# Kernel tuning notes

Hardware: AMD Instinct MI355X
Metric: run time of the kernel (lower is better)

## Reference

```python
import jax, jax.numpy as jnp
import numpy as np

NUM_PEAK = 28000
NUM_GENE = 12000
N_NODES = NUM_PEAK + NUM_GENE
N_EDGES = 640000
NUM_TOPICS = 100
T_HIDDEN = 512
EMB = 64
HID = 128  # 2 * emb_size, hidden_channels of GCN
BATCH = 256
BN_EPS = 1e-5


def setup_inputs() -> dict:
    key = jax.random.key(0)
    ks = iter(jax.random.split(key, 64))
    def nrm(shape, s=0.05):
        return jax.random.normal(next(ks), shape, dtype=jnp.float32) * s
    def unif(shape):
        return jax.random.uniform(next(ks), shape, dtype=jnp.float32)
    z = lambda *s: jnp.zeros(s, jnp.float32)
    o = lambda *s: jnp.ones(s, jnp.float32)
    inp = dict(
        Gene=unif((BATCH, NUM_GENE)),
        Gene_normalized=unif((BATCH, NUM_GENE)),
        Peak=unif((BATCH, NUM_PEAK)),
        Peak_normalized=unif((BATCH, NUM_PEAK)),
        feature_matrix=nrm((N_NODES, EMB), 1.0),
        # GATv2 layer 1 (EMB -> HID, heads=1)
        Wl1=nrm((HID, EMB)), bl1=z(HID), Wr1=nrm((HID, EMB)), br1=z(HID),
        att1=nrm((HID,), 0.1), bias1=z(HID),
        # GATv2 layer 2 (HID -> EMB)
        Wl2=nrm((EMB, HID)), bl2=z(EMB), Wr2=nrm((EMB, HID)), br2=z(EMB),
        att2=nrm((EMB,), 0.1), bias2=z(EMB),
        # gene encoder: Linear + ReLU + BN + Linear + ReLU + BN
        gW1=nrm((T_HIDDEN, NUM_GENE)), gb1=z(T_HIDDEN), gg1=o(T_HIDDEN), gbe1=z(T_HIDDEN),
        gW2=nrm((T_HIDDEN, T_HIDDEN)), gb2=z(T_HIDDEN), gg2=o(T_HIDDEN), gbe2=z(T_HIDDEN),
        # peak encoder
        pW1=nrm((T_HIDDEN, NUM_PEAK)), pb1=z(T_HIDDEN), pg1=o(T_HIDDEN), pbe1=z(T_HIDDEN),
        pW2=nrm((T_HIDDEN, T_HIDDEN)), pb2=z(T_HIDDEN), pg2=o(T_HIDDEN), pbe2=z(T_HIDDEN),
        mu_W=nrm((NUM_TOPICS, T_HIDDEN)), mu_b=z(NUM_TOPICS),
        ls_W=nrm((NUM_TOPICS, T_HIDDEN)), ls_b=z(NUM_TOPICS),
        alphas_W=nrm((NUM_TOPICS, EMB)),
        alphas_star_W=nrm((NUM_TOPICS, EMB)),
        edge_index=jax.random.randint(next(ks), (2, N_EDGES), 0, N_NODES),
    )
    return inp


def _batchnorm(h, gamma, beta):
    # training-style BN over batch axis (biased variance), eps=1e-5
    m = h.mean(axis=0)
    v = jnp.mean((h - m) ** 2, axis=0)
    return (h - m) * jax.lax.rsqrt(v + BN_EPS) * gamma + beta


def _gatv2(x, src, dst, Wl, bl, Wr, br, att, bias):
    # PyG GATv2Conv, heads=1: e_ij = att . leaky_relu(Wl x_j + Wr x_i),
    # softmax over incoming edges of i, out_i = sum_j alpha_ij * (Wl x_j) + bias
    xl = x @ Wl.T + bl            # [N, C]
    xr = x @ Wr.T + br            # [N, C]
    e = jax.nn.leaky_relu(xl[src] + xr[dst], negative_slope=0.2)  # [E, C]
    logit = e @ att               # [E]
    m = jax.ops.segment_max(logit, dst, num_segments=N_NODES)
    ex = jnp.exp(logit - m[dst])
    den = jax.ops.segment_sum(ex, dst, num_segments=N_NODES)
    alpha = ex / (den[dst] + 1e-16)
    out = jax.ops.segment_sum(alpha[:, None] * xl[src], dst, num_segments=N_NODES)
    return out + bias


def _encode(x, W1, b1, g1, be1, W2, b2, g2, be2, mu_W, mu_b, ls_W, ls_b):
    h = _batchnorm(jax.nn.relu(x @ W1.T + b1), g1, be1)
    h = _batchnorm(jax.nn.relu(h @ W2.T + b2), g2, be2)
    mu = h @ mu_W.T + mu_b
    logsigma = 2.0 * (h @ ls_W.T + ls_b)
    kl = -0.5 * jnp.sum(1.0 + logsigma - mu ** 2 - jnp.exp(logsigma), axis=-1).mean()
    return mu, kl


def reference(Gene, Gene_normalized, Peak, Peak_normalized, feature_matrix,
              Wl1, bl1, Wr1, br1, att1, bias1,
              Wl2, bl2, Wr2, br2, att2, bias2,
              gW1, gb1, gg1, gbe1, gW2, gb2, gg2, gbe2,
              pW1, pb1, pg1, pbe1, pW2, pb2, pg2, pbe2,
              mu_W, mu_b, ls_W, ls_b, alphas_W, alphas_star_W, edge_index):
    # ---- variational encoders (eval mode: dropout off, theta from mu) ----
    mu_d, kl_d = _encode(Gene_normalized, gW1, gb1, gg1, gbe1, gW2, gb2, gg2, gbe2,
                         mu_W, mu_b, ls_W, ls_b)
    mu_j, kl_j = _encode(Peak_normalized, pW1, pb1, pg1, pbe1, pW2, pb2, pg2, pbe2,
                         mu_W, mu_b, ls_W, ls_b)
    theta_d = jax.nn.softmax(mu_d, axis=-1)   # [B, K]
    theta_j = jax.nn.softmax(mu_j, axis=-1)
    kld_theta = kl_d + kl_j

    # ---- GCN embedding: two GATv2Conv layers with self-loops ----
    loops = jnp.arange(N_NODES)
    src = jnp.concatenate([edge_index[0], loops])
    dst = jnp.concatenate([edge_index[1], loops])
    h = jax.nn.relu(_gatv2(feature_matrix, src, dst, Wl1, bl1, Wr1, br1, att1, bias1))
    emb = _gatv2(h, src, dst, Wl2, bl2, Wr2, br2, att2, bias2)
    emb = jax.nn.relu(emb)  # theta_act applied in forward
    eta_matrix = emb[:NUM_PEAK]   # [num_peak, EMB]
    rho_matrix = emb[NUM_PEAK:]   # [num_gene, EMB]

    # ---- topic-word matrices: softmax over genes/peaks (dim=0), transposed ----
    beta_gene = jax.nn.softmax(rho_matrix @ alphas_W.T, axis=0).T        # [K, num_gene]
    beta_peak = jax.nn.softmax(eta_matrix @ alphas_star_W.T, axis=0).T   # [K, num_peak]

    # ---- decode + reconstruction loss ----
    preds_gene = jnp.log(theta_d @ beta_gene + 1e-6)
    preds_peak = jnp.log(theta_j @ beta_peak + 1e-6)
    recon = (-(preds_gene * Gene).sum(-1) - (preds_peak * Peak).sum(-1)).mean()
    return recon, kld_theta
```

## Files before the change

### kernel.cpp

```cpp
#include <hip/hip_runtime.h>
#include <cstdint>
#include <cstddef>

using u16 = unsigned short;
using u32 = unsigned int;
typedef __attribute__((ext_vector_type(8))) short bf16x8;
typedef __attribute__((ext_vector_type(4))) float f32x4;

static constexpr int NUM_PEAK = 28000;
static constexpr int NUM_GENE = 12000;
static constexpr int N_NODES  = NUM_PEAK + NUM_GENE;
static constexpr int N_EDGES  = 640000;
static constexpr int E_TOTAL  = N_EDGES + N_NODES;
static constexpr int NT       = 100;
static constexpr int NT2      = 200;
static constexpr int NTP      = 128;
static constexpr int TH       = 512;
static constexpr int EMB      = 64;
static constexpr int HID      = 128;
static constexpr int BATCH    = 256;
static constexpr int SCAN_CHUNK = 1024;
static constexpr int SCAN_NB  = (N_NODES + SCAN_CHUNK - 1) / SCAN_CHUNK;
static constexpr int ENC_CH   = 640;
static constexpr int KPG      = 12032;
static constexpr int KPP      = 28032;
#define BN_EPS 1e-5f

__device__ __forceinline__ u16 f2bf(float f) {
  u32 b = __float_as_uint(f);
  return (u16)((b + 0x7FFFu + ((b >> 16) & 1u)) >> 16);
}
__device__ __forceinline__ float bf2f(u16 u) {
  return __uint_as_float((u32)u << 16);
}
__device__ __forceinline__ u32 f2o(float f) {
  u32 u = __float_as_uint(f);
  return (u & 0x80000000u) ? ~u : (u | 0x80000000u);
}
__device__ __forceinline__ float o2f(u32 u) {
  return (u & 0x80000000u) ? __uint_as_float(u & 0x7fffffffu) : __uint_as_float(~u);
}

struct CvtJobs {
  const float* src[12];
  u16* dst[12];
  u32 n[12];
  u32 start[12];
  int count;
};

__global__ __launch_bounds__(256) void cvt_all(CvtJobs J) {
  const int bid = blockIdx.x;
  int seg = 0;
  while (seg + 1 < J.count && bid >= (int)J.start[seg + 1]) ++seg;
  const float* __restrict__ src = J.src[seg];
  u16* __restrict__ dst = J.dst[seg];
  const u32 n = J.n[seg];
  const u32 i = (u32)(bid - J.start[seg]) * 2048u + threadIdx.x * 8u;
  if (i + 8 <= n) {
    float4 a = *(const float4*)(src + i);
    float4 b = *(const float4*)(src + i + 4);
    ushort4 o0{f2bf(a.x), f2bf(a.y), f2bf(a.z), f2bf(a.w)};
    ushort4 o1{f2bf(b.x), f2bf(b.y), f2bf(b.z), f2bf(b.w)};
    *(ushort4*)(dst + i) = o0;
    *(ushort4*)(dst + i + 4) = o1;
  } else {
    for (u32 j = i; j < n; ++j) dst[j] = f2bf(src[j]);
  }
}

__global__ __launch_bounds__(256) void cvt_pad(
    const float* __restrict__ g, u16* __restrict__ gb,
    const float* __restrict__ p, u16* __restrict__ pb) {
  const bool sec = (blockIdx.y != 0);
  const float* __restrict__ src = sec ? p : g;
  u16* __restrict__ dst = sec ? pb : gb;
  const int K = sec ? NUM_PEAK : NUM_GENE;
  const int Kp = sec ? KPP : KPG;
  const size_t total = (size_t)BATCH * Kp;
  size_t i = ((size_t)blockIdx.x * 256 + threadIdx.x) * 8;
  const size_t stride = (size_t)gridDim.x * 256 * 8;
  for (; i < total; i += stride) {
    const int col = (int)(i % Kp);
    const size_t row = i / Kp;
    ushort4 o0{0, 0, 0, 0}, o1{0, 0, 0, 0};
    if (col + 8 <= K) {
      const float* s = src + row * K + col;
      float4 a = *(const float4*)s;
      float4 b = *(const float4*)(s + 4);
      o0 = ushort4{f2bf(a.x), f2bf(a.y), f2bf(a.z), f2bf(a.w)};
      o1 = ushort4{f2bf(b.x), f2bf(b.y), f2bf(b.z), f2bf(b.w)};
    }
    *(ushort4*)(dst + i) = o0;
    *(ushort4*)(dst + i + 4) = o1;
  }
}

struct GP {
  const u16* A; const u16* B; float* C; u16* Cb; const float* bias;
  int M, N, K, chunk;
};

__global__ __launch_bounds__(256) void gemm_bt_bf16(GP g0, GP g1, int dual) {
  const GP& g = (dual && blockIdx.z) ? g1 : g0;
  const int M = g.M, N = g.N, K = g.K;
  __shared__ u16 As[64][40];
  __shared__ u16 Bs[64][40];
  const int tid = threadIdx.x;
  const int bm = blockIdx.y * 64, bn = blockIdx.x * 64;
  if (bm >= M || bn >= N) return;
  const int k0 = dual ? 0 : blockIdx.z * g.chunk;
  const int k1 = min(K, k0 + g.chunk);
  const int w = tid >> 6, lane = tid & 63;
  const int wm = (w >> 1) * 32, wn = (w & 1) * 32;
  const int fr = lane & 15;
  const int ks = (lane >> 4) * 8;
  const int srow = tid >> 2, sseg = (tid & 3) * 8;
  f32x4 acc[2][2] = {};
  for (int kt = k0; kt < k1; kt += 32) {
    const int gk = kt + sseg;
    {
      const int gm = bm + srow;
      bf16x8 v = {0, 0, 0, 0, 0, 0, 0, 0};
      if (gm < M) {
        if (gk + 8 <= k1) v = *(const bf16x8*)(g.A + (size_t)gm * K + gk);
        else if (gk < k1)
          for (int e = 0; e < k1 - gk; ++e) ((short*)&v)[e] = (short)g.A[(size_t)gm * K + gk + e];
      }
      *(bf16x8*)&As[srow][sseg] = v;
    }
    {
      const int gn = bn + srow;
      bf16x8 v = {0, 0, 0, 0, 0, 0, 0, 0};
      if (gn < N) {
        if (gk + 8 <= k1) v = *(const bf16x8*)(g.B + (size_t)gn * K + gk);
        else if (gk < k1)
          for (int e = 0; e < k1 - gk; ++e) ((short*)&v)[e] = (short)g.B[(size_t)gn * K + gk + e];
      }
      *(bf16x8*)&Bs[srow][sseg] = v;
    }
    __syncthreads();
    bf16x8 a0 = *(const bf16x8*)&As[wm + fr][ks];
    bf16x8 a1 = *(const bf16x8*)&As[wm + 16 + fr][ks];
    bf16x8 b0 = *(const bf16x8*)&Bs[wn + fr][ks];
    bf16x8 b1 = *(const bf16x8*)&Bs[wn + 16 + fr][ks];
    acc[0][0] = __builtin_amdgcn_mfma_f32_16x16x32_bf16(a0, b0, acc[0][0], 0, 0, 0);
    acc[0][1] = __builtin_amdgcn_mfma_f32_16x16x32_bf16(a0, b1, acc[0][1], 0, 0, 0);
    acc[1][0] = __builtin_amdgcn_mfma_f32_16x16x32_bf16(a1, b0, acc[1][0], 0, 0, 0);
    acc[1][1] = __builtin_amdgcn_mfma_f32_16x16x32_bf16(a1, b1, acc[1][1], 0, 0, 0);
    __syncthreads();
  }
  const bool split = (!dual && gridDim.z > 1);
#pragma unroll
  for (int fi = 0; fi < 2; ++fi)
#pragma unroll
    for (int fj = 0; fj < 2; ++fj)
#pragma unroll
      for (int r = 0; r < 4; ++r) {
        const int row = bm + wm + fi * 16 + (lane >> 4) * 4 + r;
        const int col = bn + wn + fj * 16 + fr;
        if (row < M && col < N) {
          const float v = acc[fi][fj][r];
          if (split) atomicAdd(&g.C[(size_t)row * N + col], v);
          else if (g.Cb) g.Cb[(size_t)row * N + col] = f2bf(v + (g.bias ? g.bias[col] : 0.f));
          else g.C[(size_t)row * N + col] = v + (g.bias ? g.bias[col] : 0.f);
        }
      }
}

__device__ __forceinline__ int swz64(int row, int colu16) {
  return row * 64 + ((((colu16 >> 3) ^ row) & 7) << 3) + (colu16 & 7);
}

__global__ __launch_bounds__(256) void gemm_enc1(
    const u16* __restrict__ A0, const float* __restrict__ B0, float* __restrict__ C0,
    int K0, int Kp0, int ksp0,
    const u16* __restrict__ A1, const float* __restrict__ B1, float* __restrict__ C1,
    int K1, int Kp1) {
  const int z = blockIdx.z;
  const bool second = (z >= ksp0);
  const u16* __restrict__ A = second ? A1 : A0;
  const float* __restrict__ B = second ? B1 : B0;
  float* __restrict__ C = second ? C1 : C0;
  const int K = second ? K1 : K0;
  const int Kp = second ? Kp1 : Kp0;
  const int zz = second ? z - ksp0 : z;
  const int k0 = zz * ENC_CH;
  const int k1 = min(K, k0 + ENC_CH);
  __shared__ u16 As[128 * 64];
  __shared__ u16 Bs[64 * 64];
  const int tid = threadIdx.x;
  const int bm = blockIdx.y * 128;
  const int bn = blockIdx.x * 64;
  const int w = tid >> 6, lane = tid & 63;
  const int wm = w * 32;
  const int fr = lane & 15, g = lane >> 4;
  const int ar = tid >> 1, acol = (tid & 1) * 32;
  const int br = tid >> 2, bcol = (tid & 3) * 16;
  const u16* Abase = A + (size_t)(bm + ar) * Kp + acol;
  const float* Bbase = B + (size_t)(bn + br) * K + bcol;

  bf16x8 rA0, rA1, rA2, rA3;
  float4 rB0, rB1, rB2, rB3;
  auto LD = [&](int kt) {
    const u16* sa = Abase + kt;
    rA0 = *(const bf16x8*)(sa);
    rA1 = *(const bf16x8*)(sa + 8);
    rA2 = *(const bf16x8*)(sa + 16);
    rA3 = *(const bf16x8*)(sa + 24);
    if (kt + bcol + 16 <= K) {
      const float* sb = Bbase + kt;
      rB0 = *(const float4*)(sb);
      rB1 = *(const float4*)(sb + 4);
      rB2 = *(const float4*)(sb + 8);
      rB3 = *(const float4*)(sb + 12);
    } else {
      rB0 = float4{0.f, 0.f, 0.f, 0.f}; rB1 = rB0; rB2 = rB0; rB3 = rB0;
    }
  };
  auto ST = [&]() {
    *(bf16x8*)&As[swz64(ar, acol)] = rA0;
    *(bf16x8*)&As[swz64(ar, acol + 8)] = rA1;
    *(bf16x8*)&As[swz64(ar, acol + 16)] = rA2;
    *(bf16x8*)&As[swz64(ar, acol + 24)] = rA3;
    ushort4 p0{f2bf(rB0.x), f2bf(rB0.y), f2bf(rB0.z), f2bf(rB0.w)};
    ushort4 p1{f2bf(rB1.x), f2bf(rB1.y), f2bf(rB1.z), f2bf(rB1.w)};
    ushort4 p2{f2bf(rB2.x), f2bf(rB2.y), f2bf(rB2.z), f2bf(rB2.w)};
    ushort4 p3{f2bf(rB3.x), f2bf(rB3.y), f2bf(rB3.z), f2bf(rB3.w)};
    const int b0 = swz64(br, bcol);
    const int b1 = swz64(br, bcol + 8);
    *(ushort4*)&Bs[b0] = p0;
    *(ushort4*)&Bs[b0 + 4] = p1;
    *(ushort4*)&Bs[b1] = p2;
    *(ushort4*)&Bs[b1 + 4] = p3;
  };

  f32x4 acc[2][4] = {};
  LD(k0);
  ST();
  for (int kt = k0; kt < k1; kt += 64) {
    __syncthreads();
    const bool more = (kt + 64 < k1);
    if (more) LD(kt + 64);
#pragma unroll
    for (int s = 0; s < 2; ++s) {
      const int kc = s * 32 + g * 8;
      bf16x8 bfr[4];
#pragma unroll
      for (int fj = 0; fj < 4; ++fj)
        bfr[fj] = *(const bf16x8*)&Bs[swz64(fj * 16 + fr, kc)];
#pragma unroll
      for (int fi = 0; fi < 2; ++fi) {
        bf16x8 a = *(const bf16x8*)&As[swz64(wm + fi * 16 + fr, kc)];
#pragma unroll
        for (int fj = 0; fj < 4; ++fj)
          acc[fi][fj] = __builtin_amdgcn_mfma_f32_16x16x32_bf16(a, bfr[fj], acc[fi][fj], 0, 0, 0);
      }
    }
    __syncthreads();
    if (more) ST();
  }
#pragma unroll
  for (int fi = 0; fi < 2; ++fi)
#pragma unroll
    for (int fj = 0; fj < 4; ++fj)
#pragma unroll
      for (int r = 0; r < 4; ++r) {
        const int row = bm + wm + fi * 16 + g * 4 + r;
        const int col = bn + fj * 16 + fr;
        atomicAdd(&C[(size_t)row * TH + col], acc[fi][fj][r]);
      }
}

__global__ __launch_bounds__(256) void recon_fused(
    const u16* __restrict__ thg, const u16* __restrict__ betag,
    const float* __restrict__ Xg, int Ng, int tiles_g,
    const u16* __restrict__ thp, const u16* __restrict__ betap,
    const float* __restrict__ Xp, int Np, float* __restrict__ partials) {
  __shared__ float pred[64][65];
  __shared__ float wsum[4];
  int ct = blockIdx.x;
  const u16* A; const u16* B; const float* X; int N;
  if (ct < tiles_g) { A = thg; B = betag; X = Xg; N = Ng; }
  else { ct -= tiles_g; A = thp; B = betap; X = Xp; N = Np; }
  const int bm = blockIdx.y * 64, bn = ct * 64;
  const int tid = threadIdx.x, w = tid >> 6, lane = tid & 63;
  const int wm = (w >> 1) * 32, wn = (w & 1) * 32;
  const int fr = lane & 15, ks = (lane >> 4) * 8;
  const u16* Ar0 = A + (size_t)(bm + wm + fr) * NTP;
  const u16* Ar1 = A + (size_t)(bm + wm + 16 + fr) * NTP;
  bf16x8 a0[4], a1[4];
#pragma unroll
  for (int kt = 0; kt < 4; ++kt) {
    a0[kt] = *(const bf16x8*)(Ar0 + kt * 32 + ks);
    a1[kt] = *(const bf16x8*)(Ar1 + kt * 32 + ks);
  }
  const int gn0 = min(bn + wn + fr, N - 1);
  const int gn1 = min(bn + wn + 16 + fr, N - 1);
  const u16* Br0 = B + (size_t)gn0 * NTP;
  const u16* Br1 = B + (size_t)gn1 * NTP;
  f32x4 acc[2][2] = {};
#pragma unroll
  for (int kt = 0; kt < 4; ++kt) {
    bf16x8 b0 = *(const bf16x8*)(Br0 + kt * 32 + ks);
    bf16x8 b1 = *(const bf16x8*)(Br1 + kt * 32 + ks);
    acc[0][0] = __builtin_amdgcn_mfma_f32_16x16x32_bf16(a0[kt], b0, acc[0][0], 0, 0, 0);
    acc[0][1] = __builtin_amdgcn_mfma_f32_16x16x32_bf16(a0[kt], b1, acc[0][1], 0, 0, 0);
    acc[1][0] = __builtin_amdgcn_mfma_f32_16x16x32_bf16(a1[kt], b0, acc[1][0], 0, 0, 0);
    acc[1][1] = __builtin_amdgcn_mfma_f32_16x16x32_bf16(a1[kt], b1, acc[1][1], 0, 0, 0);
  }
#pragma unroll
  for (int fi = 0; fi < 2; ++fi)
#pragma unroll
    for (int fj = 0; fj < 2; ++fj)
#pragma unroll
      for (int r = 0; r < 4; ++r)
        pred[wm + fi * 16 + (lane >> 4) * 4 + r][wn + fj * 16 + fr] = acc[fi][fj][r];
  __syncthreads();
  float local = 0.f;
  if (bn + 64 <= N) {
#pragma unroll
    for (int k = 0; k < 4; ++k) {
      const int j = k * 1024 + tid * 4;
      const int row = j >> 6, col = j & 63;
      const float4 xv = *(const float4*)(X + (size_t)(bm + row) * N + bn + col);
      local += xv.x * __logf(pred[row][col + 0] + 1e-6f);
      local += xv.y * __logf(pred[row][col + 1] + 1e-6f);
      local += xv.z * __logf(pred[row][col + 2] + 1e-6f);
      local += xv.w * __logf(pred[row][col + 3] + 1e-6f);
    }
  } else {
#pragma unroll
    for (int k = 0; k < 16; ++k) {
      const int idx = k * 256 + tid, row = idx >> 6, col = idx & 63;
      if (bn + col < N)
        local += X[(size_t)(bm + row) * N + bn + col] * __logf(pred[row][col] + 1e-6f);
    }
  }
  for (int o = 32; o > 0; o >>= 1) local += __shfl_down(local, o);
  if (lane == 0) wsum[w] = local;
  __syncthreads();
  if (tid == 0)
    partials[(size_t)blockIdx.y * gridDim.x + blockIdx.x] =
        wsum[0] + wsum[1] + wsum[2] + wsum[3];
}

__global__ __launch_bounds__(256) void final_recon(
    const float* __restrict__ partials, int n, float* __restrict__ out) {
  float s = 0.f;
  for (int i = threadIdx.x; i < n; i += 256) s += partials[i];
  __shared__ float red[256];
  red[threadIdx.x] = s; __syncthreads();
  for (int o = 128; o > 0; o >>= 1) {
    if (threadIdx.x < o) red[threadIdx.x] += red[threadIdx.x + o];
    __syncthreads();
  }
  if (threadIdx.x == 0) out[0] = -red[0] * (1.f / BATCH);
}

__global__ __launch_bounds__(256) void bias_relu_bn2(
    const float* __restrict__ Hg, const float* __restrict__ bg,
    const float* __restrict__ gg, const float* __restrict__ beg,
    u16* __restrict__ og,
    const float* __restrict__ Hp, const float* __restrict__ bp,
    const float* __restrict__ gp, const float* __restrict__ bep,
    u16* __restrict__ op) {
  int c = blockIdx.x;
  const float *H, *b, *gma, *be; u16* ob;
  if (c < TH) { H = Hg; b = bg; gma = gg; be = beg; ob = og; }
  else { c -= TH; H = Hp; b = bp; gma = gp; be = bep; ob = op; }
  const int r = threadIdx.x;
  float v = fmaxf(H[(size_t)r * TH + c] + b[c], 0.f);
  __shared__ float red[BATCH];
  red[r] = v; __syncthreads();
  for (int s = BATCH / 2; s > 0; s >>= 1) { if (r < s) red[r] += red[r + s]; __syncthreads(); }
  const float mean = red[0] * (1.f / BATCH);
  __syncthreads();
  const float d = v - mean;
  red[r] = d * d; __syncthreads();
  for (int s = BATCH / 2; s > 0; s >>= 1) { if (r < s) red[r] += red[r + s]; __syncthreads(); }
  const float var = red[0] * (1.f / BATCH);
  ob[(size_t)r * TH + c] = f2bf(d * rsqrtf(var + BN_EPS) * gma[c] + be[c]);
}

__global__ __launch_bounds__(128) void row_kl_theta(
    const float* __restrict__ mld, const float* __restrict__ mlj,
    const float* __restrict__ mu_b, const float* __restrict__ ls_b,
    u16* __restrict__ thd, u16* __restrict__ thj, float* __restrict__ kl_out) {
  const float* ml = blockIdx.y ? mlj : mld;
  u16* thb = blockIdx.y ? thj : thd;
  const int b = blockIdx.x;
  const int t = threadIdx.x;
  const bool act = (t < NT);
  float mu = 0.f, ls = 0.f, term = 0.f;
  if (act) {
    mu = ml[(size_t)b * NT2 + t] + mu_b[t];
    ls = 2.f * (ml[(size_t)b * NT2 + NT + t] + ls_b[t]);
    term = 1.f + ls - mu * mu - expf(ls);
  }
  __shared__ float red[128];
  red[t] = act ? term : 0.f; __syncthreads();
  for (int s = 64; s > 0; s >>= 1) { if (t < s) red[t] += red[t + s]; __syncthreads(); }
  if (t == 0) atomicAdd(kl_out, -0.5f * red[0] * (1.f / BATCH));
  __syncthreads();
  red[t] = act ? mu : -INFINITY; __syncthreads();
  for (int s = 64; s > 0; s >>= 1) { if (t < s) red[t] = fmaxf(red[t], red[t + s]); __syncthreads(); }
  const float mx = red[0];
  __syncthreads();
  const float e = act ? expf(mu - mx) : 0.f;
  red[t] = e; __syncthreads();
  for (int s = 64; s > 0; s >>= 1) { if (t < s) red[t] += red[t + s]; __syncthreads(); }
  thb[(size_t)b * NTP + t] = act ? f2bf(e / red[0]) : (u16)0;
}

__global__ __launch_bounds__(256) void deg_count(
    const int* __restrict__ ei, int* __restrict__ deg) {
  int e = blockIdx.x * 256 + threadIdx.x;
  if (e >= E_TOTAL) return;
  const int d = (e < N_EDGES) ? ei[N_EDGES + e] : e - N_EDGES;
  atomicAdd(&deg[d], 1);
}

__global__ __launch_bounds__(256) void scan_part(
    const int* __restrict__ deg, int* __restrict__ bsum) {
  const int base = blockIdx.x * SCAN_CHUNK + threadIdx.x * 4;
  int s = 0;
#pragma unroll
  for (int i = 0; i < 4; ++i) {
    const int idx = base + i;
    if (idx < N_NODES) s += deg[idx];
  }
  for (int o = 32; o > 0; o >>= 1) s += __shfl_down(s, o);
  __shared__ int ws[4];
  if ((threadIdx.x & 63) == 0) ws[threadIdx.x >> 6] = s;
  __syncthreads();
  if (threadIdx.x == 0) bsum[blockIdx.x] = ws[0] + ws[1] + ws[2] + ws[3];
}

__global__ __launch_bounds__(64) void scan_bsum(int* __restrict__ bsum) {
  if (threadIdx.x == 0) {
    int run = 0;
    for (int i = 0; i < SCAN_NB; ++i) { int v = bsum[i]; bsum[i] = run; run += v; }
  }
}

__global__ __launch_bounds__(256) void scan_final(
    const int* __restrict__ deg, const int* __restrict__ bsum,
    int* __restrict__ row_ptr) {
  const int t = threadIdx.x;
  const int base = blockIdx.x * SCAN_CHUNK + t * 4;
  int v[4], s = 0;
#pragma unroll
  for (int i = 0; i < 4; ++i) {
    const int idx = base + i;
    v[i] = (idx < N_NODES) ? deg[idx] : 0;
    s += v[i];
  }
  const int lane = t & 63, w = t >> 6;
  int x = s;
  for (int o = 1; o < 64; o <<= 1) {
    int y = __shfl_up(x, o);
    if (lane >= o) x += y;
  }
  __shared__ int wtot[4];
  if (lane == 63) wtot[w] = x;
  __syncthreads();
  int woff = 0;
  for (int i = 0; i < w; ++i) woff += wtot[i];
  int excl = bsum[blockIdx.x] + woff + x - s;
#pragma unroll
  for (int i = 0; i < 4; ++i) {
    const int idx = base + i;
    if (idx < N_NODES) { row_ptr[idx] = excl; excl += v[i]; }
  }
  if (blockIdx.x == 0 && t == 0) row_ptr[N_NODES] = E_TOTAL;
}

__global__ __launch_bounds__(256) void csr_scatter(
    const int* __restrict__ ei, const int* __restrict__ row_ptr,
    int* __restrict__ cur, int* __restrict__ csr_src) {
  int e = blockIdx.x * 256 + threadIdx.x;
  if (e >= E_TOTAL) return;
  int s, d;
  if (e < N_EDGES) { s = ei[e]; d = ei[N_EDGES + e]; }
  else { s = d = e - N_EDGES; }
  const int pos = atomicAdd(&cur[d], 1);
  csr_src[row_ptr[d] + pos] = s;
}

template <int C>
__global__ __launch_bounds__(256) void gat_fused(
    const u16* __restrict__ xl, const u16* __restrict__ xr,
    const float* __restrict__ att, const float* __restrict__ bias,
    const int* __restrict__ row_ptr, const int* __restrict__ csr_src,
    u16* __restrict__ out_b) {
  constexpr int CPL = C / 8;
  constexpr int W = CPL / 2;
  const int lane = threadIdx.x & 63;
  const int g = lane >> 3, li = lane & 7;
  const int d = blockIdx.x * 4 + (threadIdx.x >> 6);
  if (d >= N_NODES) return;
  const int c0 = li * CPL;
  float xrv[CPL], attv[CPL], acc[CPL];
  {
    const u32* xrw = (const u32*)(xr + (size_t)d * C + c0);
#pragma unroll
    for (int i = 0; i < W; ++i) {
      const u32 wv = xrw[i];
      xrv[2 * i]     = __uint_as_float(wv << 16);
      xrv[2 * i + 1] = __uint_as_float(wv & 0xffff0000u);
    }
  }
#pragma unroll
  for (int i = 0; i < CPL; ++i) { attv[i] = att[c0 + i]; acc[i] = 0.f; }
  float m = -INFINITY, den = 0.f;
  const int end = row_ptr[d + 1];
  int p = row_ptr[d] + g;
  int s = (p < end) ? csr_src[p] : 0;
  u32 w[W];
  {
    const u32* sw = (const u32*)(xl + (size_t)s * C + c0);
#pragma unroll
    for (int i = 0; i < W; ++i) w[i] = sw[i];
  }
  while (p < end) {
    const int sn = (p + 8 < end) ? csr_src[p + 8] : 0;
    u32 wn[W];
    {
      const u32* sw = (const u32*)(xl + (size_t)sn * C + c0);
#pragma unroll
      for (int i = 0; i < W; ++i) wn[i] = sw[i];
    }
    float xlv[CPL];
#pragma unroll
    for (int i = 0; i < W; ++i) {
      xlv[2 * i]     = __uint_as_float(w[i] << 16);
      xlv[2 * i + 1] = __uint_as_float(w[i] & 0xffff0000u);
    }
    float part = 0.f;
#pragma unroll
    for (int i = 0; i < CPL; ++i) {
      float x = xlv[i] + xrv[i];
      x = (x > 0.f) ? x : 0.2f * x;
      part += x * attv[i];
    }
    part += __shfl_xor(part, 1);
    part += __shfl_xor(part, 2);
    part += __shfl_xor(part, 4);
    const float nm = fmaxf(m, part);
    const float scale = __expf(m - nm);
    const float ex = __expf(part - nm);
    den = den * scale + ex;
#pragma unroll
    for (int i = 0; i < CPL; ++i) acc[i] = acc[i] * scale + ex * xlv[i];
    m = nm;
    p += 8;
#pragma unroll
    for (int i = 0; i < W; ++i) w[i] = wn[i];
  }
  float M = m;
  M = fmaxf(M, __shfl_xor(M, 8));
  M = fmaxf(M, __shfl_xor(M, 16));
  M = fmaxf(M, __shfl_xor(M, 32));
  const float gs = __expf(m - M);
  den *= gs;
  den += __shfl_xor(den, 8);
  den += __shfl_xor(den, 16);
  den += __shfl_xor(den, 32);
  const float inv = 1.f / (den + 1e-16f);
  float va[CPL];
#pragma unroll
  for (int i = 0; i < CPL; ++i) {
    float a = acc[i] * gs;
    a += __shfl_xor(a, 8);
    a += __shfl_xor(a, 16);
    a += __shfl_xor(a, 32);
    va[i] = a;
  }
  if (g == 0) {
    u32* dst = (u32*)(out_b + (size_t)d * C + c0);
#pragma unroll
    for (int i = 0; i < W; ++i) {
      const u16 lo = f2bf(fmaxf(va[2 * i] * inv + bias[c0 + 2 * i], 0.f));
      const u16 hi = f2bf(fmaxf(va[2 * i + 1] * inv + bias[c0 + 2 * i + 1], 0.f));
      dst[i] = (u32)lo | ((u32)hi << 16);
    }
  }
}

__global__ __launch_bounds__(256) void init_cm(u32* __restrict__ cmax,
                                               float* __restrict__ cden) {
  const int i = threadIdx.x;
  if (i < 2 * NT) { cmax[i] = 0x007FFFFFu; cden[i] = 0.f; }
}

__global__ __launch_bounds__(256) void col_max(
    const float* __restrict__ Lg, const float* __restrict__ Lp,
    u32* __restrict__ gmx) {
  const float* L = blockIdx.y ? Lp : Lg;
  const int M = blockIdx.y ? NUM_PEAK : NUM_GENE;
  u32* mx = gmx + blockIdx.y * NT;
  const int r0 = blockIdx.x * 128;
  if (r0 >= M) return;
  __shared__ u32 s[NT];
  for (int i = threadIdx.x; i < NT; i += 256) s[i] = 0x007FFFFFu;
  __syncthreads();
  const int cnt = min(128, M - r0) * NT;
  const float* base = L + (size_t)r0 * NT;
  for (int i = threadIdx.x; i < cnt; i += 256) {
    const int c = i % NT;
    atomicMax(&s[c], f2o(base[i]));
  }
  __syncthreads();
  for (int i = threadIdx.x; i < NT; i += 256) atomicMax(&mx[i], s[i]);
}

__global__ __launch_bounds__(256) void col_sumexp(
    const float* __restrict__ Lg, const float* __restrict__ Lp,
    const u32* __restrict__ gmx, float* __restrict__ gden) {
  const float* L = blockIdx.y ? Lp : Lg;
  const int M = blockIdx.y ? NUM_PEAK : NUM_GENE;
  const u32* mxg = gmx + blockIdx.y * NT;
  float* dng = gden + blockIdx.y * NT;
  const int r0 = blockIdx.x * 128;
  if (r0 >= M) return;
  __shared__ float mx[NT];
  __shared__ float s[NT];
  for (int i = threadIdx.x; i < NT; i += 256) { mx[i] = o2f(mxg[i]); s[i] = 0.f; }
  __syncthreads();
  const int cnt = min(128, M - r0) * NT;
  const float* base = L + (size_t)r0 * NT;
  for (int i = threadIdx.x; i < cnt; i += 256) {
    const int c = i % NT;
    atomicAdd(&s[c], expf(base[i] - mx[c]));
  }
  __syncthreads();
  for (int i = threadIdx.x; i < NT; i += 256) atomicAdd(&dng[i], s[i]);
}

__global__ __launch_bounds__(256) void beta_norm(
    const float* __restrict__ Lg, const float* __restrict__ Lp,
    const u32* __restrict__ gmx, const float* __restrict__ gden,
    u16* __restrict__ og, u16* __restrict__ op) {
  const float* L = blockIdx.y ? Lp : Lg;
  const int M = blockIdx.y ? NUM_PEAK : NUM_GENE;
  const u32* mxg = gmx + blockIdx.y * NT;
  const float* dng = gden + blockIdx.y * NT;
  u16* o = blockIdx.y ? op : og;
  __shared__ float mx[NT], inv[NT];
  for (int i = threadIdx.x; i < NT; i += 256) { mx[i] = o2f(mxg[i]); inv[i] = 1.f / dng[i]; }
  __syncthreads();
  const size_t total = (size_t)M * NTP;
  size_t i = (size_t)blockIdx.x * 256 + threadIdx.x;
  const size_t stride = (size_t)gridDim.x * 256;
  for (; i < total; i += stride) {
    const int c = (int)(i & (NTP - 1));
    u16 v = 0;
    if (c < NT) {
      const size_t r = i >> 7;
      v = f2bf(expf(L[r * NT + c] - mx[c]) * inv[c]);
    }
    o[i] = v;
  }
}

extern "C" void kernel_launch(void* const* d_in, const int* in_sizes, int n_in,
                              void* d_out, int out_size, void* d_ws, size_t ws_size,
                              hipStream_t stream) {
  const float* Gene  = (const float*)d_in[0];
  const float* GeneN = (const float*)d_in[1];
  const float* Peak  = (const float*)d_in[2];
  const float* PeakN = (const float*)d_in[3];
  const float* feat  = (const float*)d_in[4];
  const float* Wl1 = (const float*)d_in[5];  const float* bl1 = (const float*)d_in[6];
  const float* Wr1 = (const float*)d_in[7];  const float* br1 = (const float*)d_in[8];
  const float* att1 = (const float*)d_in[9]; const float* bias1 = (const float*)d_in[10];
  const float* Wl2 = (const float*)d_in[11]; const float* bl2 = (const float*)d_in[12];
  const float* Wr2 = (const float*)d_in[13]; const float* br2 = (const float*)d_in[14];
  const float* att2 = (const float*)d_in[15]; const float* bias2 = (const float*)d_in[16];
  const float* gW1 = (const float*)d_in[17]; const float* gb1 = (const float*)d_in[18];
  const float* gg1 = (const float*)d_in[19]; const float* gbe1 = (const float*)d_in[20];
  const float* gW2 = (const float*)d_in[21]; const float* gb2 = (const float*)d_in[22];
  const float* gg2 = (const float*)d_in[23]; const float* gbe2 = (const float*)d_in[24];
  const float* pW1 = (const float*)d_in[25]; const float* pb1 = (const float*)d_in[26];
  const float* pg1 = (const float*)d_in[27]; const float* pbe1 = (const float*)d_in[28];
  const float* pW2 = (const float*)d_in[29]; const float* pb2 = (const float*)d_in[30];
  const float* pg2 = (const float*)d_in[31]; const float* pbe2 = (const float*)d_in[32];
  const float* mu_W = (const float*)d_in[33]; const float* mu_b = (const float*)d_in[34];
  const float* ls_W = (const float*)d_in[35]; const float* ls_b = (const float*)d_in[36];
  const float* alphas_W = (const float*)d_in[37];
  const float* alphas_star_W = (const float*)d_in[38];
  const int* ei = (const int*)d_in[39];
  float* out = (float*)d_out;
  (void)in_sizes; (void)n_in; (void)ws_size;

  char* base = (char*)d_ws;
  size_t off = 0;
  auto A = [&](size_t bytes) { void* p = base + off; off += (bytes + 255) & ~(size_t)255; return p; };
  int* deg     = (int*)A((size_t)N_NODES * 4);
  int* cur     = (int*)A((size_t)N_NODES * 4);
  int* row_ptr = (int*)A((size_t)(N_NODES + 1) * 4);
  int* bsum    = (int*)A((size_t)(SCAN_NB + 1) * 4);
  int* csr_src = (int*)A((size_t)E_TOTAL * 4);
  float* h1g = (float*)A((size_t)BATCH * TH * 4);
  float* h1p = (float*)A((size_t)BATCH * TH * 4);
  float* h2g = (float*)A((size_t)BATCH * TH * 4);
  float* h2p = (float*)A((size_t)BATCH * TH * 4);
  u16* h1gb = (u16*)A((size_t)BATCH * TH * 2);
  u16* h2gb = (u16*)A((size_t)BATCH * TH * 2);
  u16* h1pb = (u16*)A((size_t)BATCH * TH * 2);
  u16* h2pb = (u16*)A((size_t)BATCH * TH * 2);
  float* ml_d = (float*)A((size_t)BATCH * NT2 * 4);
  float* ml_j = (float*)A((size_t)BATCH * NT2 * 4);
  u16* th_db = (u16*)A((size_t)BATCH * NTP * 2);
  u16* th_jb = (u16*)A((size_t)BATCH * NTP * 2);
  float* lgg = (float*)A((size_t)NUM_GENE * NT * 4);
  float* lgp = (float*)A((size_t)NUM_PEAK * NT * 4);
  u16* betagb = (u16*)A((size_t)NUM_GENE * NTP * 2);
  u16* betapb = (u16*)A((size_t)NUM_PEAK * NTP * 2);
  u16* featb = (u16*)A((size_t)N_NODES * EMB * 2);
  u16* gW2b = (u16*)A((size_t)TH * TH * 2);
  u16* pW2b = (u16*)A((size_t)TH * TH * 2);
  u16* mlWb = (u16*)A((size_t)NT2 * TH * 2);
  u16* Wl1b = (u16*)A((size_t)HID * EMB * 2);
  u16* Wr1b = (u16*)A((size_t)HID * EMB * 2);
  u16* Wl2b = (u16*)A((size_t)EMB * HID * 2);
  u16* Wr2b = (u16*)A((size_t)EMB * HID * 2);
  u16* aWb  = (u16*)A((size_t)NT * EMB * 2);
  u16* aSWb = (u16*)A((size_t)NT * EMB * 2);
  u16* agg1b = (u16*)A((size_t)N_NODES * HID * 2);
  u16* embb  = (u16*)A((size_t)N_NODES * EMB * 2);
  u32* cmax = (u32*)A(2 * NT * 4);
  float* cden = (float*)A(2 * NT * 4);
  float* partials = (float*)A(4096 * 4);
  u16* xl1b = (u16*)A((size_t)N_NODES * HID * 2);
  u16* xr1b = (u16*)A((size_t)N_NODES * HID * 2);
  u16* xl2b = (u16*)A((size_t)N_NODES * EMB * 2);
  u16* xr2b = (u16*)A((size_t)N_NODES * EMB * 2);
  u16* GeneNb = (u16*)A((size_t)BATCH * KPG * 2);
  u16* PeakNb = (u16*)A((size_t)BATCH * KPP * 2);

  auto cdiv = [](int a, int b) { return (a + b - 1) / b; };
  auto Z = [&](void* p, size_t bytes) { hipMemsetAsync(p, 0, bytes, stream); };

  Z(d_out, (size_t)out_size * sizeof(float));
  Z(deg, 2 * (size_t)N_NODES * 4);

  deg_count<<<cdiv(E_TOTAL, 256), 256, 0, stream>>>(ei, deg);
  scan_part<<<SCAN_NB, 256, 0, stream>>>(deg, bsum);
  scan_bsum<<<1, 64, 0, stream>>>(bsum);
  scan_final<<<SCAN_NB, 256, 0, stream>>>(deg, bsum, row_ptr);
  csr_scatter<<<cdiv(E_TOTAL, 256), 256, 0, stream>>>(ei, row_ptr, cur, csr_src);

  {
    const int blocks = cdiv(BATCH * KPP / 8, 256);
    cvt_pad<<<dim3(blocks, 2), 256, 0, stream>>>(GeneN, GeneNb, PeakN, PeakNb);
  }

  {
    CvtJobs J = {};
    int c = 0; u32 blocks = 0;
    auto add = [&](const float* s, u16* d, size_t n) {
      J.src[c] = s; J.dst[c] = d; J.n[c] = (u32)n; J.start[c] = blocks;
      blocks += (u32)((n + 2047) / 2048); ++c;
    };
    add(gW2, gW2b, (size_t)TH * TH);
    add(pW2, pW2b, (size_t)TH * TH);
    add(mu_W, mlWb, (size_t)NT * TH);
    add(ls_W, mlWb + (size_t)NT * TH, (size_t)NT * TH);
    add(feat, featb, (size_t)N_NODES * EMB);
    add(Wl1, Wl1b, (size_t)HID * EMB);
    add(Wr1, Wr1b, (size_t)HID * EMB);
    add(Wl2, Wl2b, (size_t)EMB * HID);
    add(Wr2, Wr2b, (size_t)EMB * HID);
    add(alphas_W, aWb, (size_t)NT * EMB);
    add(alphas_star_W, aSWb, (size_t)NT * EMB);
    J.count = c;
    cvt_all<<<blocks, 256, 0, stream>>>(J);
  }

  const int kspG = cdiv(NUM_GENE, ENC_CH);
  const int kspP = cdiv(NUM_PEAK, ENC_CH);
  Z(h1g, 2 * (size_t)BATCH * TH * 4);
  gemm_enc1<<<dim3(TH / 64, BATCH / 128, kspG + kspP), 256, 0, stream>>>(
      GeneNb, gW1, h1g, NUM_GENE, KPG, kspG,
      PeakNb, pW1, h1p, NUM_PEAK, KPP);
  bias_relu_bn2<<<2 * TH, BATCH, 0, stream>>>(h1g, gb1, gg1, gbe1, h1gb,
                                              h1p, pb1, pg1, pbe1, h1pb);
  {
    GP g = {h1gb, gW2b, h2g, nullptr, nullptr, BATCH, TH, TH, TH};
    GP p = {h1pb, pW2b, h2p, nullptr, nullptr, BATCH, TH, TH, TH};
    gemm_bt_bf16<<<dim3(TH / 64, BATCH / 64, 2), 256, 0, stream>>>(g, p, 1);
  }
  bias_relu_bn2<<<2 * TH, BATCH, 0, stream>>>(h2g, gb2, gg2, gbe2, h2gb,
                                              h2p, pb2, pg2, pbe2, h2pb);
  {
    GP g = {h2gb, mlWb, ml_d, nullptr, nullptr, BATCH, NT2, TH, TH};
    GP p = {h2pb, mlWb, ml_j, nullptr, nullptr, BATCH, NT2, TH, TH};
    gemm_bt_bf16<<<dim3(cdiv(NT2, 64), BATCH / 64, 2), 256, 0, stream>>>(g, p, 1);
  }
  row_kl_theta<<<dim3(BATCH, 2), 128, 0, stream>>>(ml_d, ml_j, mu_b, ls_b, th_db, th_jb, out + 1);

  {
    GP l = {featb, Wl1b, nullptr, xl1b, bl1, N_NODES, HID, EMB, EMB};
    GP r = {featb, Wr1b, nullptr, xr1b, br1, N_NODES, HID, EMB, EMB};
    gemm_bt_bf16<<<dim3(HID / 64, N_NODES / 64, 2), 256, 0, stream>>>(l, r, 1);
  }
  gat_fused<HID><<<N_NODES / 4, 256, 0, stream>>>(xl1b, xr1b, att1, bias1, row_ptr, csr_src, agg1b);

  {
    GP l = {agg1b, Wl2b, nullptr, xl2b, bl2, N_NODES, EMB, HID, HID};
    GP r = {agg1b, Wr2b, nullptr, xr2b, br2, N_NODES, EMB, HID, HID};
    gemm_bt_bf16<<<dim3(EMB / 64, N_NODES / 64, 2), 256, 0, stream>>>(l, r, 1);
  }
  gat_fused<EMB><<<N_NODES / 4, 256, 0, stream>>>(xl2b, xr2b, att2, bias2, row_ptr, csr_src, embb);

  {
    GP g = {embb + (size_t)NUM_PEAK * EMB, aWb, lgg, nullptr, nullptr, NUM_GENE, NT, EMB, EMB};
    GP p = {embb, aSWb, lgp, nullptr, nullptr, NUM_PEAK, NT, EMB, EMB};
    gemm_bt_bf16<<<dim3(2, cdiv(NUM_PEAK, 64), 2), 256, 0, stream>>>(g, p, 1);
  }
  init_cm<<<1, 256, 0, stream>>>(cmax, cden);
  col_max<<<dim3(cdiv(NUM_PEAK, 128), 2), 256, 0, stream>>>(lgg, lgp, cmax);
  col_sumexp<<<dim3(cdiv(NUM_PEAK, 128), 2), 256, 0, stream>>>(lgg, lgp, cmax, cden);
  beta_norm<<<dim3(1024, 2), 256, 0, stream>>>(lgg, lgp, cmax, cden, betagb, betapb);

  const int tiles_g = cdiv(NUM_GENE, 64);
  const int tiles_p = cdiv(NUM_PEAK, 64);
  const int tiles = tiles_g + tiles_p;
  recon_fused<<<dim3(tiles, 4), 256, 0, stream>>>(
      th_db, betagb, Gene, NUM_GENE, tiles_g,
      th_jb, betapb, Peak, NUM_PEAK, partials);
  final_recon<<<1, 256, 0, stream>>>(partials, tiles * 4, out);
}
```

Baseline: 410.9 us.

## Replace column max/sum-exp atomics with online-softmax partials and remap encoder GEMM blocks

```diff
diff --git a/kernel.cpp b/kernel.cpp
--- a/kernel.cpp
+++ b/kernel.cpp
@@ -24,6 +24,8 @@
 static constexpr int ENC_CH   = 640;
 static constexpr int KPG      = 12032;
 static constexpr int KPP      = 28032;
+static constexpr int CS_ROWS  = 128;
+static constexpr int NBMAX    = (NUM_PEAK + CS_ROWS - 1) / CS_ROWS;
 #define BN_EPS 1e-5f
 
 __device__ __forceinline__ u16 f2bf(float f) {
@@ -32,13 +34,6 @@
 }
 __device__ __forceinline__ float bf2f(u16 u) {
   return __uint_as_float((u32)u << 16);
-}
-__device__ __forceinline__ u32 f2o(float f) {
-  u32 u = __float_as_uint(f);
-  return (u & 0x80000000u) ? ~u : (u | 0x80000000u);
-}
-__device__ __forceinline__ float o2f(u32 u) {
-  return (u & 0x80000000u) ? __uint_as_float(u & 0x7fffffffu) : __uint_as_float(~u);
 }
 
 struct CvtJobs {
@@ -177,21 +172,33 @@
     int K0, int Kp0, int ksp0,
     const u16* __restrict__ A1, const float* __restrict__ B1, float* __restrict__ C1,
     int K1, int Kp1) {
-  const int z = blockIdx.z;
-  const bool second = (z >= ksp0);
+  int bx = blockIdx.x, by = blockIdx.y, bz = blockIdx.z;
+  {
+    const int gx = gridDim.x, gy = gridDim.y;
+    const int nwg = gx * gy * gridDim.z;
+    if ((nwg & 7) == 0) {
+      const int f = bx + gx * (by + gy * bz);
+      const int cpx = nwg >> 3;
+      const int f2 = (f & 7) * cpx + (f >> 3);
+      bx = f2 % gx;
+      by = (f2 / gx) % gy;
+      bz = f2 / (gx * gy);
+    }
+  }
+  const bool second = (bz >= ksp0);
   const u16* __restrict__ A = second ? A1 : A0;
   const float* __restrict__ B = second ? B1 : B0;
   float* __restrict__ C = second ? C1 : C0;
   const int K = second ? K1 : K0;
   const int Kp = second ? Kp1 : Kp0;
-  const int zz = second ? z - ksp0 : z;
+  const int zz = second ? bz - ksp0 : bz;
   const int k0 = zz * ENC_CH;
   const int k1 = min(K, k0 + ENC_CH);
   __shared__ u16 As[128 * 64];
   __shared__ u16 Bs[64 * 64];
   const int tid = threadIdx.x;
-  const int bm = blockIdx.y * 128;
-  const int bn = blockIdx.x * 64;
+  const int bm = by * 128;
+  const int bn = bx * 64;
   const int w = tid >> 6, lane = tid & 63;
   const int wm = w * 32;
   const int fr = lane & 15, g = lane >> 4;
@@ -588,67 +595,63 @@
   }
 }
 
-__global__ __launch_bounds__(256) void init_cm(u32* __restrict__ cmax,
-                                               float* __restrict__ cden) {
-  const int i = threadIdx.x;
-  if (i < 2 * NT) { cmax[i] = 0x007FFFFFu; cden[i] = 0.f; }
-}
-
-__global__ __launch_bounds__(256) void col_max(
+__global__ __launch_bounds__(128) void col_stats(
     const float* __restrict__ Lg, const float* __restrict__ Lp,
-    u32* __restrict__ gmx) {
-  const float* L = blockIdx.y ? Lp : Lg;
-  const int M = blockIdx.y ? NUM_PEAK : NUM_GENE;
-  u32* mx = gmx + blockIdx.y * NT;
-  const int r0 = blockIdx.x * 128;
-  if (r0 >= M) return;
-  __shared__ u32 s[NT];
-  for (int i = threadIdx.x; i < NT; i += 256) s[i] = 0x007FFFFFu;
-  __syncthreads();
-  const int cnt = min(128, M - r0) * NT;
-  const float* base = L + (size_t)r0 * NT;
-  for (int i = threadIdx.x; i < cnt; i += 256) {
-    const int c = i % NT;
-    atomicMax(&s[c], f2o(base[i]));
-  }
-  __syncthreads();
-  for (int i = threadIdx.x; i < NT; i += 256) atomicMax(&mx[i], s[i]);
-}
-
-__global__ __launch_bounds__(256) void col_sumexp(
-    const float* __restrict__ Lg, const float* __restrict__ Lp,
-    const u32* __restrict__ gmx, float* __restrict__ gden) {
-  const float* L = blockIdx.y ? Lp : Lg;
-  const int M = blockIdx.y ? NUM_PEAK : NUM_GENE;
-  const u32* mxg = gmx + blockIdx.y * NT;
-  float* dng = gden + blockIdx.y * NT;
-  const int r0 = blockIdx.x * 128;
-  if (r0 >= M) return;
-  __shared__ float mx[NT];
-  __shared__ float s[NT];
-  for (int i = threadIdx.x; i < NT; i += 256) { mx[i] = o2f(mxg[i]); s[i] = 0.f; }
-  __syncthreads();
-  const int cnt = min(128, M - r0) * NT;
-  const float* base = L + (size_t)r0 * NT;
-  for (int i = threadIdx.x; i < cnt; i += 256) {
-    const int c = i % NT;
-    atomicAdd(&s[c], expf(base[i] - mx[c]));
-  }
-  __syncthreads();
-  for (int i = threadIdx.x; i < NT; i += 256) atomicAdd(&dng[i], s[i]);
+    float* __restrict__ bstats) {
+  const bool sec = (blockIdx.y != 0);
+  const float* L = sec ? Lp : Lg;
+  const int M = sec ? NUM_PEAK : NUM_GENE;
+  const int r0 = blockIdx.x * CS_ROWS;
+  const int c = threadIdx.x;
+  float* bs = bstats + (((size_t)blockIdx.y * NBMAX + blockIdx.x) * NT + (c < NT ? c : 0)) * 2;
+  if (r0 >= M) {
+    if (c < NT) { bs[0] = -INFINITY; bs[1] = 0.f; }
+    return;
+  }
+  if (c >= NT) return;
+  const int rend = min(r0 + CS_ROWS, M);
+  float m = -INFINITY, s = 0.f;
+  for (int r = r0; r < rend; ++r) {
+    const float v = L[(size_t)r * NT + c];
+    const float nm = fmaxf(m, v);
+    s = s * __expf(m - nm) + __expf(v - nm);
+    m = nm;
+  }
+  bs[0] = m;
+  bs[1] = s;
+}
+
+__global__ __launch_bounds__(128) void col_merge(
+    const float* __restrict__ bstats, int nbG, int nbP,
+    float* __restrict__ mstat, float* __restrict__ istat) {
+  const bool sec = (blockIdx.y != 0);
+  const int nb = sec ? nbP : nbG;
+  const int c = threadIdx.x;
+  if (c >= NT) return;
+  const float* bs = bstats + ((size_t)blockIdx.y * NBMAX * NT + c) * 2;
+  float M = -INFINITY, S = 0.f;
+  for (int b = 0; b < nb; ++b) {
+    const float mb = bs[(size_t)b * NT * 2];
+    const float sb = bs[(size_t)b * NT * 2 + 1];
+    const float nm = fmaxf(M, mb);
+    S = S * __expf(M - nm) + sb * __expf(mb - nm);
+    M = nm;
+  }
+  mstat[blockIdx.y * NT + c] = M;
+  istat[blockIdx.y * NT + c] = 1.f / S;
 }
 
 __global__ __launch_bounds__(256) void beta_norm(
     const float* __restrict__ Lg, const float* __restrict__ Lp,
-    const u32* __restrict__ gmx, const float* __restrict__ gden,
+    const float* __restrict__ mstat, const float* __restrict__ istat,
     u16* __restrict__ og, u16* __restrict__ op) {
   const float* L = blockIdx.y ? Lp : Lg;
   const int M = blockIdx.y ? NUM_PEAK : NUM_GENE;
-  const u32* mxg = gmx + blockIdx.y * NT;
-  const float* dng = gden + blockIdx.y * NT;
+  const float* mxg = mstat + blockIdx.y * NT;
+  const float* ivg = istat + blockIdx.y * NT;
   u16* o = blockIdx.y ? op : og;
   __shared__ float mx[NT], inv[NT];
-  for (int i = threadIdx.x; i < NT; i += 256) { mx[i] = o2f(mxg[i]); inv[i] = 1.f / dng[i]; }
+  for (int i = threadIdx.x; i < NT; i += 256) { mx[i] = mxg[i]; inv[i] = ivg[i]; }
   __syncthreads();
   const size_t total = (size_t)M * NTP;
   size_t i = (size_t)blockIdx.x * 256 + threadIdx.x;
@@ -658,7 +661,7 @@
     u16 v = 0;
     if (c < NT) {
       const size_t r = i >> 7;
-      v = f2bf(expf(L[r * NT + c] - mx[c]) * inv[c]);
+      v = f2bf(__expf(L[r * NT + c] - mx[c]) * inv[c]);
     }
     o[i] = v;
   }
@@ -730,8 +733,9 @@
   u16* aSWb = (u16*)A((size_t)NT * EMB * 2);
   u16* agg1b = (u16*)A((size_t)N_NODES * HID * 2);
   u16* embb  = (u16*)A((size_t)N_NODES * EMB * 2);
-  u32* cmax = (u32*)A(2 * NT * 4);
-  float* cden = (float*)A(2 * NT * 4);
+  float* mstat = (float*)A(2 * NT * 4);
+  float* istat = (float*)A(2 * NT * 4);
+  float* bstats = (float*)A((size_t)2 * NBMAX * NT * 2 * 4);
   float* partials = (float*)A(4096 * 4);
   u16* xl1b = (u16*)A((size_t)N_NODES * HID * 2);
   u16* xr1b = (u16*)A((size_t)N_NODES * HID * 2);
@@ -820,10 +824,11 @@
     GP p = {embb, aSWb, lgp, nullptr, nullptr, NUM_PEAK, NT, EMB, EMB};
     gemm_bt_bf16<<<dim3(2, cdiv(NUM_PEAK, 64), 2), 256, 0, stream>>>(g, p, 1);
   }
-  init_cm<<<1, 256, 0, stream>>>(cmax, cden);
-  col_max<<<dim3(cdiv(NUM_PEAK, 128), 2), 256, 0, stream>>>(lgg, lgp, cmax);
-  col_sumexp<<<dim3(cdiv(NUM_PEAK, 128), 2), 256, 0, stream>>>(lgg, lgp, cmax, cden);
-  beta_norm<<<dim3(1024, 2), 256, 0, stream>>>(lgg, lgp, cmax, cden, betagb, betapb);
+  const int nbG = cdiv(NUM_GENE, CS_ROWS);
+  const int nbP = cdiv(NUM_PEAK, CS_ROWS);
+  col_stats<<<dim3(NBMAX, 2), 128, 0, stream>>>(lgg, lgp, bstats);
+  col_merge<<<dim3(1, 2), 128, 0, stream>>>(bstats, nbG, nbP, mstat, istat);
+  beta_norm<<<dim3(1024, 2), 256, 0, stream>>>(lgg, lgp, mstat, istat, betagb, betapb);
 
   const int tiles_g = cdiv(NUM_GENE, 64);
   const int tiles_p = cdiv(NUM_PEAK, 64);
```

After: 442.0 us. 7.5% more time.
